# Kernel tuning notes

Measured on AMD Instinct MI355X. Metric: run time of the kernel, lower is better.

The kernel has to match this reference:

```python
import jax, jax.numpy as jnp
import numpy as np

N, IN_FEAT, OUT_FEAT, H = 4096, 256, 256, 8
D = OUT_FEAT // H  # per-head dim = 32
ADJ_DENSITY = 0.05


def setup_inputs() -> dict:
    key = jax.random.key(0)
    kx, kw, kb, ka, kadj = jax.random.split(key, 5)
    x = jax.random.normal(kx, (N, IN_FEAT), dtype=jnp.float32)
    # eqx.nn.Linear params: weight [out, in], bias [out]
    W = jax.random.normal(kw, (OUT_FEAT, IN_FEAT), dtype=jnp.float32) * (1.0 / np.sqrt(IN_FEAT))
    b = jax.random.normal(kb, (OUT_FEAT,), dtype=jnp.float32) * 0.01
    a = jax.random.normal(ka, (H, 2 * D), dtype=jnp.float32)
    adj_matrix = jax.random.bernoulli(kadj, ADJ_DENSITY, (N, N)).astype(jnp.float32)
    return {"x": x, "W": W, "b": b, "a": a, "adj_matrix": adj_matrix}


def reference(x, W, b, a, adj_matrix):
    num_nodes = x.shape[0]
    num_heads = a.shape[0]
    half = a.shape[1] // 2
    # projection: [N, H*D] -> [N, H, D]
    node_feats = (x @ W.T + b).reshape(num_nodes, num_heads, half)
    # per-head additive attention halves -> [N, H]
    logit_parent = (node_feats * a[None, :, :half]).sum(axis=-1)
    logit_child = (node_feats * a[None, :, half:]).sum(axis=-1)
    # [N, N, H] dense logits via broadcast-add
    attn_logits = logit_parent[:, None, :] + logit_child[None, :, :]
    attn_logits = jax.nn.leaky_relu(attn_logits, 0.2)
    # NOTE: faithful to source — masked entries set to 0.0 (not -inf)
    attn_logits = jnp.where(jnp.abs(adj_matrix)[..., None] != 0.0, attn_logits, 0.0)
    attn_probs = jax.nn.softmax(attn_logits, axis=1)
    out = jnp.einsum('ijh,jhc->ihc', attn_probs, node_feats)
    return out.reshape(num_nodes, -1)
```

## Files before the change

### kernel.cpp

```cpp
#include <hip/hip_runtime.h>

#define NN    4096
#define OF    256
#define NH    8
#define MAXNZ 384

typedef __attribute__((ext_vector_type(8))) short short8;
typedef __attribute__((ext_vector_type(4))) float f32x4;

__device__ __forceinline__ float bf2f(unsigned int u) {
    union { unsigned int i; float f; } v; v.i = u << 16; return v.f;
}
__device__ __forceinline__ unsigned short f2bf(float f) {
    union { float f; unsigned int i; } v; v.f = f;
    unsigned int x = v.i;
    return (unsigned short)((x + 0x7fffu + ((x >> 16) & 1u)) >> 16);
}
__device__ __forceinline__ unsigned int pk2bf(float a, float b) {
    return (unsigned int)f2bf(a) | ((unsigned int)f2bf(b) << 16);
}

__global__ __launch_bounds__(256) void k_pre(
    const float* __restrict__ adjf, const float* __restrict__ Wf,
    int* __restrict__ flag, unsigned short* __restrict__ Wbh,
    unsigned short* __restrict__ Wbl, float* __restrict__ zbase)
{
    __shared__ int viol;
    int t = threadIdx.x;
    int gid = blockIdx.x * 256 + t;
    if (t == 0) viol = 0;
    __syncthreads();
    int bad = 0;
    for (int k = t; k < NN; k += 256) {
        float v = adjf[k];
        if (!(v == 0.0f || v == 1.0f)) bad = 1;
    }
    if (bad) atomicAdd(&viol, 1);
    __syncthreads();
    int f = viol > 0;
    if (t == 0) *flag = f;

    zbase[gid] = 0.f;
    if (gid < 256) zbase[65536 + gid] = 0.f;
    if (!f) {
        float v = Wf[gid];
        unsigned short h = f2bf(v);
        Wbh[gid] = h; Wbl[gid] = f2bf(v - bf2f(h));
    }
}

__global__ __launch_bounds__(256) void k_proj(
    const void* __restrict__ xraw, const void* __restrict__ Wraw,
    const void* __restrict__ braw, const void* __restrict__ araw,
    const int* __restrict__ flag,
    const unsigned short* __restrict__ Wbh, const unsigned short* __restrict__ Wbl,
    unsigned short* __restrict__ nfb, float* __restrict__ lp,
    float* __restrict__ lc, float* __restrict__ Stot)
{
    __shared__ unsigned short xh[16][264], xl[16][264];

    int f = *flag;
    int t = threadIdx.x;
    int wave = t >> 6;
    int lane = t & 63;
    int pid = blockIdx.x;

    int tid  = pid * 4 + wave;
    int mt = tid >> 4, nt = tid & 15;
    int lr = lane & 15;
    int kq = (lane >> 4) * 8;

    if (!f) {
        const float* xsrc = (const float*)xraw + (size_t)mt * 4096;
        #pragma unroll
        for (int q = 0; q < 16; q++) {
            int e = t + 256*q;
            float v = xsrc[e];
            unsigned short h = f2bf(v);
            xh[e >> 8][e & 255] = h;
            xl[e >> 8][e & 255] = f2bf(v - bf2f(h));
        }
        __syncthreads();
    }

    size_t wo = (size_t)(nt*16 + lr)*OF + kq;
    f32x4 acc = {0.f, 0.f, 0.f, 0.f};
    if (f) {
        const short8* xp = reinterpret_cast<const short8*>(
            (const unsigned short*)xraw + (size_t)(mt*16 + lr)*OF + kq);
        const short8* wp = reinterpret_cast<const short8*>(
            (const unsigned short*)Wraw + wo);
        #pragma unroll
        for (int kk = 0; kk < OF/32; kk++)
            acc = __builtin_amdgcn_mfma_f32_16x16x32_bf16(xp[kk*4], wp[kk*4], acc, 0, 0, 0);
    } else {
        const short8* wh = reinterpret_cast<const short8*>(Wbh + wo);
        const short8* wl = reinterpret_cast<const short8*>(Wbl + wo);
        #pragma unroll
        for (int kk = 0; kk < OF/32; kk++) {
            short8 ah = *reinterpret_cast<const short8*>(&xh[lr][kk*32 + kq]);
            short8 al = *reinterpret_cast<const short8*>(&xl[lr][kk*32 + kq]);
            short8 bh = wh[kk*4], bl = wl[kk*4];
            acc = __builtin_amdgcn_mfma_f32_16x16x32_bf16(ah, bh, acc, 0, 0, 0);
            acc = __builtin_amdgcn_mfma_f32_16x16x32_bf16(ah, bl, acc, 0, 0, 0);
            acc = __builtin_amdgcn_mfma_f32_16x16x32_bf16(al, bh, acc, 0, 0, 0);
        }
    }

    int col  = nt*16 + lr;
    int row0 = mt*16 + (lane >> 4) * 4;
    int h = col >> 5, cc = col & 31;
    float bias, apar, achd;
    if (f) {
        bias = bf2f((unsigned int)((const unsigned short*)braw)[col]);
        apar = bf2f((unsigned int)((const unsigned short*)araw)[h*64 + cc]);
        achd = bf2f((unsigned int)((const unsigned short*)araw)[h*64 + 32 + cc]);
    } else {
        bias = ((const float*)braw)[col];
        apar = ((const float*)araw)[h*64 + cc];
        achd = ((const float*)araw)[h*64 + 32 + cc];
    }
    float st = 0.f, pr[4], cr[4];
    #pragma unroll
    for (int r = 0; r < 4; r++) {
        float v = acc[r] + bias;
        nfb[(size_t)(row0 + r) * OF + col] = f2bf(v);
        st += v;
        pr[r] = v * apar;
        cr[r] = v * achd;
    }
    #pragma unroll
    for (int m = 1; m <= 8; m <<= 1) {
        #pragma unroll
        for (int r = 0; r < 4; r++) {
            pr[r] += __shfl_xor(pr[r], m, 64);
            cr[r] += __shfl_xor(cr[r], m, 64);
        }
    }
    if ((lane & 15) == 0) {
        #pragma unroll
        for (int r = 0; r < 4; r++) {
            atomicAdd(&lp[(row0 + r) * NH + h], pr[r]);
            atomicAdd(&lc[(row0 + r) * NH + h], cr[r]);
        }
    }
    st += __shfl_down(st, 16, 64);
    st += __shfl_down(st, 32, 64);
    if (lane < 16) atomicAdd(&Stot[col], st);
}

__global__ __launch_bounds__(256, 8) void k_attn(
    const int* __restrict__ flag, const float* __restrict__ adjf,
    const float* __restrict__ lp, const float* __restrict__ lc,
    const unsigned short* __restrict__ nfb, const float* __restrict__ Stot,
    void* __restrict__ outv)
{
    __shared__ float lps[NH];
    __shared__ int   jro[MAXNZ];
    __shared__ float wlist[MAXNZ][NH];
    __shared__ float zred[256];
    __shared__ float gred[3][256];
    __shared__ int   wtot[4];

    int i = blockIdx.x;
    int t = threadIdx.x;
    int lane = t & 63, wid = t >> 6;
    int f = *flag;
    if (t < NH) lps[t] = lp[i*NH + t];

    unsigned int m16 = 0;
    if (f) {
        const uint4* ap = reinterpret_cast<const uint4*>(
            (const unsigned short*)adjf + (size_t)i * NN + wid * 1024);
        #pragma unroll
        for (int g = 0; g < 2; g++) {
            uint4 v = ap[lane + 64*g];
            unsigned int wd[4] = {v.x, v.y, v.z, v.w};
            #pragma unroll
            for (int u = 0; u < 4; u++) {
                if (wd[u] & 0xffffu) m16 |= 1u << (g*8 + 2*u);
                if (wd[u] >> 16)     m16 |= 1u << (g*8 + 2*u + 1);
            }
        }
    } else {
        const uint4* ap = reinterpret_cast<const uint4*>(
            adjf + (size_t)i * NN + wid * 1024);
        #pragma unroll
        for (int g = 0; g < 4; g++) {
            uint4 v = ap[lane + 64*g];
            if (v.x) m16 |= 1u << (g*4);
            if (v.y) m16 |= 1u << (g*4 + 1);
            if (v.z) m16 |= 1u << (g*4 + 2);
            if (v.w) m16 |= 1u << (g*4 + 3);
        }
    }

    int pc = __popc(m16);
    int pref = pc;
    #pragma unroll
    for (int off = 1; off < 64; off <<= 1) {
        int u = __shfl_up(pref, off, 64);
        if (lane >= off) pref += u;
    }
    if (lane == 63) wtot[wid] = pref;
    __syncthreads();
    int w0 = wtot[0], w1 = wtot[1], w2 = wtot[2], w3 = wtot[3];
    int n = min(w0 + w1 + w2 + w3, MAXNZ);
    int base = (wid > 0 ? w0 : 0) + (wid > 1 ? w1 : 0) + (wid > 2 ? w2 : 0);
    int pos = base + pref - pc;
    unsigned int mm = m16;
    int jb = wid * 1024;
    while (mm && pos < MAXNZ) {
        int q = __builtin_ctz(mm);
        mm &= mm - 1;
        int j = f ? (jb + lane*8 + ((q >> 3) << 9) + (q & 7))
                  : (jb + lane*4 + ((q >> 2) << 8) + (q & 3));
        jro[pos++] = j * OF;
    }
    __syncthreads();

    int h8 = t & 7, c32 = t >> 3;
    float lph = lps[h8];
    float zp = 0.f;
    int k3 = c32;
    for (; k3 + 32 < n; k3 += 64) {
        int j0 = jro[k3] >> 5, j1 = jro[k3 + 32] >> 5;
        float l0 = lc[j0 + h8], l1 = lc[j1 + h8];
        float s0 = lph + l0; s0 = s0 > 0.f ? s0 : 0.2f * s0;
        float s1 = lph + l1; s1 = s1 > 0.f ? s1 : 0.2f * s1;
        float w0 = __expf(fminf(s0, 70.f)) - 1.f;
        float w1 = __expf(fminf(s1, 70.f)) - 1.f;
        wlist[k3][h8] = w0; wlist[k3 + 32][h8] = w1;
        zp += w0 + w1;
    }
    if (k3 < n) {
        float s = lph + lc[(jro[k3] >> 5) + h8];
        s = s > 0.f ? s : 0.2f * s;
        float w = __expf(fminf(s, 70.f)) - 1.f;
        wlist[k3][h8] = w;
        zp += w;
    }
    zred[t] = zp;
    __syncthreads();

    int hh = lane >> 3;
    int c4 = lane * 4;
    float a0 = 0.f, a1 = 0.f, a2 = 0.f, a3 = 0.f;
    int k = wid;
    for (; k + 28 < n; k += 32) {
        int jj[8]; float ww[8];
        #pragma unroll
        for (int u = 0; u < 8; u++) {
            jj[u] = __builtin_amdgcn_readfirstlane(jro[k + 4*u]);
            ww[u] = wlist[k + 4*u][hh];
        }
        uint2 d[8];
        #pragma unroll
        for (int u = 0; u < 8; u++)
            d[u] = *reinterpret_cast<const uint2*>(nfb + jj[u] + c4);
        #pragma unroll
        for (int u = 0; u < 8; u++) {
            a0 += ww[u] * bf2f(d[u].x & 0xffffu);
            a1 += ww[u] * bf2f(d[u].x >> 16);
            a2 += ww[u] * bf2f(d[u].y & 0xffffu);
            a3 += ww[u] * bf2f(d[u].y >> 16);
        }
    }
    for (; k < n; k += 4) {
        int j = __builtin_amdgcn_readfirstlane(jro[k]);
        float w = wlist[k][hh];
        uint2 d = *reinterpret_cast<const uint2*>(nfb + j + c4);
        a0 += w * bf2f(d.x & 0xffffu);
        a1 += w * bf2f(d.x >> 16);
        a2 += w * bf2f(d.y & 0xffffu);
        a3 += w * bf2f(d.y >> 16);
    }
    if (wid) {
        gred[wid-1][c4]   = a0; gred[wid-1][c4+1] = a1;
        gred[wid-1][c4+2] = a2; gred[wid-1][c4+3] = a3;
    }
    __syncthreads();

    if (wid == 0) {
        float z = zred[lane] + zred[lane+64] + zred[lane+128] + zred[lane+192];
        z += __shfl_down(z, 32, 64);
        z += __shfl_down(z, 16, 64);
        z += __shfl_down(z, 8, 64);
        float zfull = __shfl(z, hh, 64);
        float iz = 1.0f / (4096.0f + zfull);
        a0 += gred[0][c4]   + gred[1][c4]   + gred[2][c4];
        a1 += gred[0][c4+1] + gred[1][c4+1] + gred[2][c4+1];
        a2 += gred[0][c4+2] + gred[1][c4+2] + gred[2][c4+2];
        a3 += gred[0][c4+3] + gred[1][c4+3] + gred[2][c4+3];
        float4 stv = *reinterpret_cast<const float4*>(Stot + c4);
        float o0 = (stv.x + a0) * iz;
        float o1 = (stv.y + a1) * iz;
        float o2 = (stv.z + a2) * iz;
        float o3 = (stv.w + a3) * iz;
        if (f) {
            uint2 pk; pk.x = pk2bf(o0, o1); pk.y = pk2bf(o2, o3);
            *reinterpret_cast<uint2*>((unsigned short*)outv + (size_t)i*OF + c4) = pk;
        } else {
            float4 o = {o0, o1, o2, o3};
            *reinterpret_cast<float4*>((float*)outv + (size_t)i*OF + c4) = o;
        }
    }
}

extern "C" void kernel_launch(void* const* d_in, const int* in_sizes, int n_in,
                              void* d_out, int out_size, void* d_ws, size_t ws_size,
                              hipStream_t stream) {
    const void* x   = d_in[0];
    const void* W   = d_in[1];
    const void* b   = d_in[2];
    const void* a   = d_in[3];
    const void* adj = d_in[4];

    char* ws = (char*)d_ws;
    const size_t MB = 1024u*1024u, KB = 1024u;
    unsigned short* nfb  = (unsigned short*)(ws);
    float*          lp   = (float*)(ws + 2*MB);
    float*          lc   = (float*)(ws + 2*MB + 128*KB);
    float*          Stot = (float*)(ws + 2*MB + 256*KB);
    int*            flag = (int*)(ws + 2*MB + 257*KB);
    unsigned short* Wbh  = (unsigned short*)(ws + 6*MB);
    unsigned short* Wbl  = (unsigned short*)(ws + 6*MB + 128*KB);

    k_pre  <<<256,  256, 0, stream>>>((const float*)adj, (const float*)W,
                                      flag, Wbh, Wbl, lp);
    k_proj <<<1024, 256, 0, stream>>>(x, W, b, a, flag, Wbh, Wbl,
                                      nfb, lp, lc, Stot);
    k_attn <<<NN,   256, 0, stream>>>(flag, (const float*)adj, lp, lc,
                                      nfb, Stot, d_out);
}
```

Measured before the change: 154.1 us.

## Split attention rows across two blocks with atomic partials and a finalize kernel

Each output row is now handled by two blocks, each covering half of the adjacency columns. The blocks accumulate partial weighted sums and softmax denominators into fp32 workspace buffers with atomics. A new finalize kernel then applies the normalization and writes the output. The goal is more parallelism and lower per-block latency and shared memory, at the cost of zeroing 4 MB of partials, extra atomic traffic and one more kernel launch.

```diff
diff --git a/kernel.cpp b/kernel.cpp
--- a/kernel.cpp
+++ b/kernel.cpp
@@ -1,9 +1,9 @@
 #include <hip/hip_runtime.h>
 
-#define NN    4096
-#define OF    256
-#define NH    8
-#define MAXNZ 384
+#define NN     4096
+#define OF     256
+#define NH     8
+#define MAXNZH 192
 
 typedef __attribute__((ext_vector_type(8))) short short8;
 typedef __attribute__((ext_vector_type(4))) float f32x4;
@@ -23,7 +23,8 @@
 __global__ __launch_bounds__(256) void k_pre(
     const float* __restrict__ adjf, const float* __restrict__ Wf,
     int* __restrict__ flag, unsigned short* __restrict__ Wbh,
-    unsigned short* __restrict__ Wbl, float* __restrict__ zbase)
+    unsigned short* __restrict__ Wbl, float* __restrict__ zbase,
+    float* __restrict__ outP, float* __restrict__ zP)
 {
     __shared__ int viol;
     int t = threadIdx.x;
@@ -42,6 +43,10 @@
 
     zbase[gid] = 0.f;
     if (gid < 256) zbase[65536 + gid] = 0.f;
+    #pragma unroll
+    for (int e = 0; e < 16; e++)
+        outP[(size_t)gid + 65536u*e] = 0.f;
+    if (gid < 32768) zP[gid] = 0.f;
     if (!f) {
         float v = Wf[gid];
         unsigned short h = f2bf(v);
@@ -152,50 +157,50 @@
 __global__ __launch_bounds__(256, 8) void k_attn(
     const int* __restrict__ flag, const float* __restrict__ adjf,
     const float* __restrict__ lp, const float* __restrict__ lc,
-    const unsigned short* __restrict__ nfb, const float* __restrict__ Stot,
-    void* __restrict__ outv)
+    const unsigned short* __restrict__ nfb,
+    float* __restrict__ outP, float* __restrict__ zP)
 {
     __shared__ float lps[NH];
-    __shared__ int   jro[MAXNZ];
-    __shared__ float wlist[MAXNZ][NH];
+    __shared__ int   jro[MAXNZH];
+    __shared__ float wlist[MAXNZH][NH];
     __shared__ float zred[256];
     __shared__ float gred[3][256];
     __shared__ int   wtot[4];
 
-    int i = blockIdx.x;
+    int bid  = blockIdx.x;
+    int i    = bid >> 1;
+    int half = bid & 1;
     int t = threadIdx.x;
     int lane = t & 63, wid = t >> 6;
     int f = *flag;
     if (t < NH) lps[t] = lp[i*NH + t];
 
-    unsigned int m16 = 0;
+    int jb = half*2048 + wid*512;
+    unsigned int m8 = 0;
     if (f) {
         const uint4* ap = reinterpret_cast<const uint4*>(
-            (const unsigned short*)adjf + (size_t)i * NN + wid * 1024);
+            (const unsigned short*)adjf + (size_t)i * NN + jb);
+        uint4 v = ap[lane];
+        unsigned int wd[4] = {v.x, v.y, v.z, v.w};
+        #pragma unroll
+        for (int u = 0; u < 4; u++) {
+            if (wd[u] & 0xffffu) m8 |= 1u << (2*u);
+            if (wd[u] >> 16)     m8 |= 1u << (2*u + 1);
+        }
+    } else {
+        const uint4* ap = reinterpret_cast<const uint4*>(
+            adjf + (size_t)i * NN + jb);
         #pragma unroll
         for (int g = 0; g < 2; g++) {
             uint4 v = ap[lane + 64*g];
-            unsigned int wd[4] = {v.x, v.y, v.z, v.w};
-            #pragma unroll
-            for (int u = 0; u < 4; u++) {
-                if (wd[u] & 0xffffu) m16 |= 1u << (g*8 + 2*u);
-                if (wd[u] >> 16)     m16 |= 1u << (g*8 + 2*u + 1);
-            }
-        }
-    } else {
-        const uint4* ap = reinterpret_cast<const uint4*>(
-            adjf + (size_t)i * NN + wid * 1024);
-        #pragma unroll
-        for (int g = 0; g < 4; g++) {
-            uint4 v = ap[lane + 64*g];
-            if (v.x) m16 |= 1u << (g*4);
-            if (v.y) m16 |= 1u << (g*4 + 1);
-            if (v.z) m16 |= 1u << (g*4 + 2);
-            if (v.w) m16 |= 1u << (g*4 + 3);
-        }
-    }
-
-    int pc = __popc(m16);
+            if (v.x) m8 |= 1u << (g*4);
+            if (v.y) m8 |= 1u << (g*4 + 1);
+            if (v.z) m8 |= 1u << (g*4 + 2);
+            if (v.w) m8 |= 1u << (g*4 + 3);
+        }
+    }
+
+    int pc = __popc(m8);
     int pref = pc;
     #pragma unroll
     for (int off = 1; off < 64; off <<= 1) {
@@ -205,15 +210,14 @@
     if (lane == 63) wtot[wid] = pref;
     __syncthreads();
     int w0 = wtot[0], w1 = wtot[1], w2 = wtot[2], w3 = wtot[3];
-    int n = min(w0 + w1 + w2 + w3, MAXNZ);
+    int n = min(w0 + w1 + w2 + w3, MAXNZH);
     int base = (wid > 0 ? w0 : 0) + (wid > 1 ? w1 : 0) + (wid > 2 ? w2 : 0);
     int pos = base + pref - pc;
-    unsigned int mm = m16;
-    int jb = wid * 1024;
-    while (mm && pos < MAXNZ) {
+    unsigned int mm = m8;
+    while (mm && pos < MAXNZH) {
         int q = __builtin_ctz(mm);
         mm &= mm - 1;
-        int j = f ? (jb + lane*8 + ((q >> 3) << 9) + (q & 7))
+        int j = f ? (jb + lane*8 + q)
                   : (jb + lane*4 + ((q >> 2) << 8) + (q & 3));
         jro[pos++] = j * OF;
     }
@@ -286,24 +290,42 @@
         z += __shfl_down(z, 32, 64);
         z += __shfl_down(z, 16, 64);
         z += __shfl_down(z, 8, 64);
-        float zfull = __shfl(z, hh, 64);
-        float iz = 1.0f / (4096.0f + zfull);
+        if (lane < 8) atomicAdd(&zP[i*NH + lane], z);
         a0 += gred[0][c4]   + gred[1][c4]   + gred[2][c4];
         a1 += gred[0][c4+1] + gred[1][c4+1] + gred[2][c4+1];
         a2 += gred[0][c4+2] + gred[1][c4+2] + gred[2][c4+2];
         a3 += gred[0][c4+3] + gred[1][c4+3] + gred[2][c4+3];
-        float4 stv = *reinterpret_cast<const float4*>(Stot + c4);
-        float o0 = (stv.x + a0) * iz;
-        float o1 = (stv.y + a1) * iz;
-        float o2 = (stv.z + a2) * iz;
-        float o3 = (stv.w + a3) * iz;
-        if (f) {
-            uint2 pk; pk.x = pk2bf(o0, o1); pk.y = pk2bf(o2, o3);
-            *reinterpret_cast<uint2*>((unsigned short*)outv + (size_t)i*OF + c4) = pk;
-        } else {
-            float4 o = {o0, o1, o2, o3};
-            *reinterpret_cast<float4*>((float*)outv + (size_t)i*OF + c4) = o;
-        }
+        float* op = outP + (size_t)i * OF + c4;
+        atomicAdd(op,     a0);
+        atomicAdd(op + 1, a1);
+        atomicAdd(op + 2, a2);
+        atomicAdd(op + 3, a3);
+    }
+}
+
+__global__ __launch_bounds__(256) void k_fin(
+    const int* __restrict__ flag, const float* __restrict__ outP,
+    const float* __restrict__ zP, const float* __restrict__ Stot,
+    void* __restrict__ outv)
+{
+    int t = threadIdx.x;
+    int row = blockIdx.x * 4 + (t >> 6);
+    int c4 = (t & 63) * 4;
+    int f = *flag;
+    float4 p  = *reinterpret_cast<const float4*>(outP + (size_t)row*OF + c4);
+    float4 st = *reinterpret_cast<const float4*>(Stot + c4);
+    float z = zP[row*NH + (c4 >> 5)];
+    float iz = 1.0f / (4096.0f + z);
+    float o0 = (st.x + p.x) * iz;
+    float o1 = (st.y + p.y) * iz;
+    float o2 = (st.z + p.z) * iz;
+    float o3 = (st.w + p.w) * iz;
+    if (f) {
+        uint2 pk; pk.x = pk2bf(o0, o1); pk.y = pk2bf(o2, o3);
+        *reinterpret_cast<uint2*>((unsigned short*)outv + (size_t)row*OF + c4) = pk;
+    } else {
+        float4 o = {o0, o1, o2, o3};
+        *reinterpret_cast<float4*>((float*)outv + (size_t)row*OF + c4) = o;
     }
 }
 
@@ -323,13 +345,16 @@
     float*          lc   = (float*)(ws + 2*MB + 128*KB);
     float*          Stot = (float*)(ws + 2*MB + 256*KB);
     int*            flag = (int*)(ws + 2*MB + 257*KB);
-    unsigned short* Wbh  = (unsigned short*)(ws + 6*MB);
-    unsigned short* Wbl  = (unsigned short*)(ws + 6*MB + 128*KB);
+    float*          zP   = (float*)(ws + 2*MB + 258*KB);
+    unsigned short* Wbh  = (unsigned short*)(ws + 2*MB + 386*KB);
+    unsigned short* Wbl  = (unsigned short*)(ws + 2*MB + 514*KB);
+    float*          outP = (float*)(ws + 2*MB + 642*KB);
 
     k_pre  <<<256,  256, 0, stream>>>((const float*)adj, (const float*)W,
-                                      flag, Wbh, Wbl, lp);
+                                      flag, Wbh, Wbl, lp, outP, zP);
     k_proj <<<1024, 256, 0, stream>>>(x, W, b, a, flag, Wbh, Wbl,
                                       nfb, lp, lc, Stot);
-    k_attn <<<NN,   256, 0, stream>>>(flag, (const float*)adj, lp, lc,
-                                      nfb, Stot, d_out);
-}
+    k_attn <<<8192, 256, 0, stream>>>(flag, (const float*)adj, lp, lc,
+                                      nfb, outP, zP);
+    k_fin  <<<1024, 256, 0, stream>>>(flag, outP, zP, Stot, d_out);
+}
```

New measurement: 167.6 us. 8.7% more time.
